# Kernel optimization log

Measured on AMD Instinct MI355X. Metric: run time of the kernel, lower is better.

## Reference

```python
import jax, jax.numpy as jnp
import numpy as np

N_NODES = 100000
NEG_SLOPE = 0.2


def _gat_conv(x, edge_index, W, att_src, att_dst, bias):
    """Single-head PyG-style GATConv with self-loops.
    x: [N, F_in], edge_index: [2, E] (row 0 = src j, row 1 = dst i).
    """
    N = x.shape[0]
    h = x @ W  # [N, F_out]
    # add self-loops
    loop = jnp.arange(N, dtype=edge_index.dtype)
    src = jnp.concatenate([edge_index[0], loop])
    dst = jnp.concatenate([edge_index[1], loop])
    # per-node attention terms, gathered per edge
    a_s = h @ att_src  # [N]
    a_d = h @ att_dst  # [N]
    e = jax.nn.leaky_relu(a_s[src] + a_d[dst], NEG_SLOPE)  # [E+N]
    # segment softmax over incoming edges of each destination
    m = jax.ops.segment_max(e, dst, num_segments=N)  # [N]
    m = jnp.where(jnp.isfinite(m), m, 0.0)
    p = jnp.exp(e - m[dst])
    denom = jax.ops.segment_sum(p, dst, num_segments=N)  # [N], >0 due to self-loops
    alpha = p / denom[dst]  # [E+N]
    # scatter-aggregate weighted source features
    out = jax.ops.segment_sum(h[src] * alpha[:, None], dst, num_segments=N)
    return out + bias


def setup_inputs() -> dict:
    key = jax.random.key(0)
    ks = jax.random.split(key, 12)
    F_in, H, C = 128, 64, 40
    x = jax.random.normal(ks[0], (N_NODES, F_in), dtype=jnp.float32)
    edge_index = jax.random.randint(ks[1], (2, 1600000), 0, N_NODES, dtype=jnp.int64)
    s1 = 1.0 / np.sqrt(F_in)
    s2 = 1.0 / np.sqrt(H)
    return {
        "x": x,
        "edge_index": edge_index,
        "W1": jax.random.uniform(ks[2], (F_in, H), jnp.float32, -s1, s1),
        "att_src1": jax.random.uniform(ks[3], (H,), jnp.float32, -s2, s2),
        "att_dst1": jax.random.uniform(ks[4], (H,), jnp.float32, -s2, s2),
        "b1": jnp.zeros((H,), jnp.float32),
        "W2": jax.random.uniform(ks[5], (H, C), jnp.float32, -s2, s2),
        "att_src2": jax.random.uniform(ks[6], (C,), jnp.float32, -1.0 / np.sqrt(C), 1.0 / np.sqrt(C)),
        "att_dst2": jax.random.uniform(ks[7], (C,), jnp.float32, -1.0 / np.sqrt(C), 1.0 / np.sqrt(C)),
        "b2": jnp.zeros((C,), jnp.float32),
    }


def reference(x, edge_index, W1, att_src1, att_dst1, b1, W2, att_src2, att_dst2, b2):
    h = _gat_conv(x, edge_index, W1, att_src1, att_dst1, b1)
    h = jax.nn.relu(h)
    # dropout is identity in eval mode
    out = _gat_conv(h, edge_index, W2, att_src2, att_dst2, b2)
    return out
```

## Files before the change

kernel.cpp:

```cpp
#include <hip/hip_runtime.h>
#include <math.h>


#define NEG_SLOPE 0.2f
#define BIN_SHIFT 8
#define BIN_NODES 256
#define MAXBINS   512
#define CAPB      4864
#define K1_CHUNK  4096
#define MAXDEG    128
#define AGG_STRIDE 132
#define XS1 136

typedef _Float16 h4_t __attribute__((ext_vector_type(4)));
typedef _Float16 h8_t __attribute__((ext_vector_type(8)));
typedef float    f16x_t __attribute__((ext_vector_type(16)));

__device__ __forceinline__ float lrelu(float v) {
    return v > 0.f ? v : NEG_SLOPE * v;
}

__global__ __launch_bounds__(256) void prep_kernel(
    const float* __restrict__ W1, const float* __restrict__ W2,
    const float* __restrict__ as1, const float* __restrict__ ad1,
    const float* __restrict__ as2, const float* __restrict__ ad2,
    _Float16* __restrict__ w1t, _Float16* __restrict__ w2t,
    float* __restrict__ u1, float* __restrict__ v1,
    int* __restrict__ bin_cursor)
{
    const int tid = threadIdx.x;
    if (blockIdx.x == 0) {
        for (int j = tid; j < MAXBINS; j += 256) bin_cursor[j] = 0;
        for (int i = tid; i < 8192; i += 256) {
            int n = i >> 7, k = i & 127;
            w1t[i] = (_Float16)W1[k * 64 + n];
        }
        if (tid < 128) {
            float su = 0.f, sv = 0.f;
            for (int n = 0; n < 64; ++n) {
                float w = W1[tid * 64 + n];
                su += w * as1[n];
                sv += w * ad1[n];
            }
            u1[tid] = su; v1[tid] = sv;
        }
    } else {
        __shared__ float u2l[64], v2l[64];
        if (tid < 64) {
            float su = 0.f, sv = 0.f;
            for (int n = 0; n < 40; ++n) {
                float w = W2[tid * 40 + n];
                su += w * as2[n];
                sv += w * ad2[n];
            }
            u2l[tid] = su; v2l[tid] = sv;
        }
        __syncthreads();
        for (int i = tid; i < 4096; i += 256) {
            int n = i >> 6, k = i & 63;
            _Float16 o = (_Float16)0.f;
            if (n < 40)       o = (_Float16)W2[k * 40 + n];
            else if (n == 40) o = (_Float16)u2l[k];
            else if (n == 41) o = (_Float16)v2l[k];
            w2t[i] = o;
        }
    }
}

__global__ __launch_bounds__(256) void gemm1_bin_kernel(
    const float* __restrict__ x, const _Float16* __restrict__ w1t,
    const float* __restrict__ u1, const float* __restrict__ v1,
    _Float16* __restrict__ h, float* __restrict__ as_, float* __restrict__ ad_,
    int N, int gb,
    const int* __restrict__ src, const int* __restrict__ dst, int E, int nbins,
    int* __restrict__ bin_cursor, int* __restrict__ binned)
{
    __shared__ __align__(16) char smem[35840];
    const int tid = threadIdx.x;

    if (blockIdx.x < gb) {
        _Float16* Xs = (_Float16*)smem;
        _Float16* Wt = (_Float16*)(smem + 17408);
        float*    Us = (float*)(smem + 34816);
        float*    Vs = (float*)(smem + 35328);
        const int lane = tid & 63;
        const int w = tid >> 6;
        const int rh = w >> 1, ch = w & 1;
        const long rowbase = (long)blockIdx.x * 64;

        {
            const int4* s4 = (const int4*)w1t;
#pragma unroll
            for (int i = 0; i < 4; ++i) {
                int f = tid + i * 256;
                int n = f >> 4, c = f & 15;
                *(int4*)&Wt[n * XS1 + c * 8] = s4[f];
            }
        }
        {
            const float4* X4 = (const float4*)x;
            const long gmax = (long)N * 32;
#pragma unroll
            for (int i = 0; i < 8; ++i) {
                int f = tid + i * 256;
                int row = f >> 5, c4 = f & 31;
                long gi = (rowbase + row) * 32 + c4;
                float4 v = (gi < gmax) ? X4[gi] : make_float4(0.f, 0.f, 0.f, 0.f);
                h4_t hv;
                hv.x = (_Float16)v.x; hv.y = (_Float16)v.y;
                hv.z = (_Float16)v.z; hv.w = (_Float16)v.w;
                *(h4_t*)&Xs[row * XS1 + c4 * 4] = hv;
            }
        }
        if (tid < 128) Us[tid] = u1[tid];
        else { int t = tid - 128; Vs[t] = v1[t]; }
        __syncthreads();

        {
            const int arow = tid >> 2, apart = tid & 3;
            const _Float16* xr = &Xs[arow * XS1 + apart * 32];
            float ps = 0.f, pd = 0.f;
#pragma unroll
            for (int k = 0; k < 32; k += 4) {
                h4_t xv = *(const h4_t*)(xr + k);
                float4 uu = *(const float4*)&Us[apart * 32 + k];
                float4 vv = *(const float4*)&Vs[apart * 32 + k];
                float x0 = (float)xv.x, x1 = (float)xv.y, x2 = (float)xv.z, x3 = (float)xv.w;
                ps += x0 * uu.x + x1 * uu.y + x2 * uu.z + x3 * uu.w;
                pd += x0 * vv.x + x1 * vv.y + x2 * vv.z + x3 * vv.w;
            }
            ps += __shfl_xor(ps, 1); ps += __shfl_xor(ps, 2);
            pd += __shfl_xor(pd, 1); pd += __shfl_xor(pd, 2);
            if (apart == 0 && rowbase + arow < N) {
                as_[rowbase + arow] = ps;
                ad_[rowbase + arow] = pd;
            }
        }

        const int m = lane & 31, khalf = lane >> 5;
        const _Float16* ax = &Xs[(rh * 32 + m) * XS1 + khalf * 8];
        const _Float16* bx = &Wt[(ch * 32 + m) * XS1 + khalf * 8];

        f16x_t acc = {};
#pragma unroll
        for (int kc = 0; kc < 8; ++kc) {
            h8_t a = *(const h8_t*)(ax + kc * 16);
            h8_t b = *(const h8_t*)(bx + kc * 16);
            acc = __builtin_amdgcn_mfma_f32_32x32x16_f16(a, b, acc, 0, 0, 0);
        }

        const int col = ch * 32 + m;
#pragma unroll
        for (int r = 0; r < 16; ++r) {
            int rowl = (r & 3) + 8 * (r >> 2) + 4 * khalf;
            long grow = rowbase + rh * 32 + rowl;
            if (grow < N) h[grow * 64 + col] = (_Float16)acc[r];
        }
    } else {
        int* hist = (int*)smem;
        int* base = (int*)(smem + 2048);
        int* lcur = (int*)(smem + 4096);
        const int e0 = (blockIdx.x - gb) * K1_CHUNK;

        int sreg[16], dreg[16];
#pragma unroll
        for (int k = 0; k < 16; ++k) {
            int e = e0 + tid + k * 256;
            bool ok = e < E;
            dreg[k] = ok ? dst[e] : -1;
            sreg[k] = ok ? src[e] : 0;
        }

        for (int j = tid; j < nbins; j += 256) hist[j] = 0;
        __syncthreads();
#pragma unroll
        for (int k = 0; k < 16; ++k)
            if (dreg[k] >= 0) atomicAdd(&hist[dreg[k] >> BIN_SHIFT], 1);
        __syncthreads();
        for (int j = tid; j < nbins; j += 256) {
            int c = hist[j];
            base[j] = (c > 0) ? atomicAdd(&bin_cursor[j], c) : 0;
            lcur[j] = 0;
        }
        __syncthreads();
#pragma unroll
        for (int k = 0; k < 16; ++k) {
            if (dreg[k] >= 0) {
                int b = dreg[k] >> BIN_SHIFT;
                int o = atomicAdd(&lcur[b], 1);
                int pos = base[b] + o;
                if (pos < CAPB)
                    binned[b * CAPB + pos] =
                        (sreg[k] << BIN_SHIFT) | (dreg[k] & (BIN_NODES - 1));
            }
        }
    }
}

__global__ __launch_bounds__(512) void fine_kernel(
    const int* __restrict__ bin_cursor, const int* __restrict__ binned,
    int* __restrict__ csr, int* __restrict__ rowptr, int N, int nbins)
{
    __shared__ int a[MAXBINS];
    __shared__ int nh[BIN_NODES];
    __shared__ int cur[BIN_NODES];
    __shared__ int sb[2];
    const int b = blockIdx.x;
    const int tid = threadIdx.x;

    int v = (tid < nbins) ? min(bin_cursor[tid], CAPB) : 0;
    a[tid] = v;
    __syncthreads();
#pragma unroll
    for (int ofs = 1; ofs < MAXBINS; ofs <<= 1) {
        int t = (tid >= ofs) ? a[tid - ofs] : 0;
        __syncthreads();
        a[tid] += t;
        __syncthreads();
    }
    if (tid == 0) {
        sb[0] = (b > 0) ? a[b - 1] : 0;
        sb[1] = a[nbins - 1];
    }

    const int cnt = min(bin_cursor[b], CAPB);
    const int nn = min(BIN_NODES, N - b * BIN_NODES);
    const int* __restrict__ brec = binned + (long)b * CAPB;

    if (tid < BIN_NODES) nh[tid] = 0;
    __syncthreads();

    for (int k = tid; k < cnt; k += 512) {
        atomicAdd(&nh[brec[k] & (BIN_NODES - 1)], 1);
    }
    __syncthreads();

    int hv = (tid < BIN_NODES) ? nh[tid] : 0;
#pragma unroll
    for (int ofs = 1; ofs < BIN_NODES; ofs <<= 1) {
        int t = (tid >= ofs && tid < BIN_NODES) ? nh[tid - ofs] : 0;
        __syncthreads();
        if (tid < BIN_NODES) nh[tid] += t;
        __syncthreads();
    }
    const int binbase = sb[0];
    if (tid < BIN_NODES) {
        int excl = nh[tid] - hv;
        if (tid < nn) rowptr[b * BIN_NODES + tid] = binbase + excl;
        cur[tid] = binbase + excl;
    }
    if (b == nbins - 1 && tid == 0) rowptr[N] = sb[1];
    __syncthreads();

    for (int k = tid; k < cnt; k += 512) {
        int rec = brec[k];
        int pos = atomicAdd(&cur[rec & (BIN_NODES - 1)], 1);
        csr[pos] = rec >> BIN_SHIFT;
    }
}

#define XS2 72
__global__ __launch_bounds__(256) void gemm2_kernel(
    const _Float16* __restrict__ hin, const _Float16* __restrict__ w2t,
    _Float16* __restrict__ h2, float* __restrict__ as_, float* __restrict__ ad_,
    int N)
{
    __shared__ __align__(16) _Float16 Xs[64 * XS2];
    __shared__ __align__(16) _Float16 Wt[64 * XS2];
    const int tid = threadIdx.x;
    const int lane = tid & 63;
    const int w = tid >> 6;
    const int rh = w >> 1, ch = w & 1;
    const long rowbase = (long)blockIdx.x * 64;

    {
        const int4* s4 = (const int4*)w2t;
#pragma unroll
        for (int i = 0; i < 2; ++i) {
            int f = tid + i * 256;
            int n = f >> 3, c = f & 7;
            *(int4*)&Wt[n * XS2 + c * 8] = s4[f];
        }
    }
    {
        const h8_t* X8 = (const h8_t*)hin;
        const long gmax = (long)N * 8;
#pragma unroll
        for (int i = 0; i < 2; ++i) {
            int f = tid + i * 256;
            int row = f >> 3, c = f & 7;
            long gi = (rowbase + row) * 8 + c;
            h8_t v = {};
            if (gi < gmax) v = X8[gi];
#pragma unroll
            for (int j = 0; j < 8; ++j) v[j] = (v[j] > (_Float16)0.f) ? v[j] : (_Float16)0.f;
            *(h8_t*)&Xs[row * XS2 + c * 8] = v;
        }
    }
    __syncthreads();

    const int m = lane & 31, khalf = lane >> 5;
    const _Float16* ax = &Xs[(rh * 32 + m) * XS2 + khalf * 8];
    const _Float16* bx = &Wt[(ch * 32 + m) * XS2 + khalf * 8];

    f16x_t acc = {};
#pragma unroll
    for (int kc = 0; kc < 4; ++kc) {
        h8_t a = *(const h8_t*)(ax + kc * 16);
        h8_t b = *(const h8_t*)(bx + kc * 16);
        acc = __builtin_amdgcn_mfma_f32_32x32x16_f16(a, b, acc, 0, 0, 0);
    }

    const int col = ch * 32 + m;
#pragma unroll
    for (int r = 0; r < 16; ++r) {
        int rowl = (r & 3) + 8 * (r >> 2) + 4 * khalf;
        long grow = rowbase + rh * 32 + rowl;
        float v = acc[r];
        if (grow < N) {
            if (col < 40)       h2[grow * 40 + col] = (_Float16)v;
            else if (col == 40) as_[grow] = v;
            else if (col == 41) ad_[grow] = v;
        }
    }
}

template<int F, typename OT>
__global__ __launch_bounds__(256) void aggregate_kernel(
    const _Float16* __restrict__ h, const float* __restrict__ as_,
    const float* __restrict__ ad_, const int* __restrict__ rowptr,
    const int* __restrict__ csr, const float* __restrict__ bias,
    OT* __restrict__ out, int N)
{
    __shared__ __align__(16) int   Ss[16 * AGG_STRIDE];
    __shared__ __align__(16) float Ps[16 * AGG_STRIDE];
    const int tid = threadIdx.x;
    const int dl  = tid >> 4;
    const int sub = tid & 15;
    const int i = blockIdx.x * 16 + dl;
    const bool alive = (i < N);

    int r0 = 0, deg = 0;
    if (alive) {
        r0 = rowptr[i];
        deg = rowptr[i + 1] - r0;
        if (deg > MAXDEG) deg = MAXDEG;
    }
    const float adi    = alive ? ad_[i] : 0.f;
    const float e_self = alive ? lrelu(as_[i] + adi) : 0.f;

    int*   __restrict__ sp = &Ss[dl * AGG_STRIDE];
    float* __restrict__ pp = &Ps[dl * AGG_STRIDE];

    float psum = 0.f;
    for (int c = sub; c < deg; c += 16) {
        int s = csr[r0 + c];
        float p = __expf(lrelu(as_[s] + adi));
        sp[c] = s;
        pp[c] = p;
        psum += p;
    }
#pragma unroll
    for (int off = 1; off < 16; off <<= 1) psum += __shfl_xor(psum, off);
    const float p_self = __expf(e_self);
    const float inv = 1.f / (psum + p_self);

    const bool act = (sub * 4 < F);
    const int  col = act ? sub * 4 : 0;
    float4 acc = make_float4(0.f, 0.f, 0.f, 0.f);

    int k = 0;
    for (; k + 8 <= deg; k += 8) {
        int4   s0 = *(const int4*)&sp[k];
        int4   s1 = *(const int4*)&sp[k + 4];
        float4 p0 = *(const float4*)&pp[k];
        float4 p1 = *(const float4*)&pp[k + 4];
        if (act) {
            h4_t hA = *(const h4_t*)&h[(long)s0.x * F + col];
            h4_t hB = *(const h4_t*)&h[(long)s0.y * F + col];
            h4_t hC = *(const h4_t*)&h[(long)s0.z * F + col];
            h4_t hD = *(const h4_t*)&h[(long)s0.w * F + col];
            h4_t hE = *(const h4_t*)&h[(long)s1.x * F + col];
            h4_t hF = *(const h4_t*)&h[(long)s1.y * F + col];
            h4_t hG = *(const h4_t*)&h[(long)s1.z * F + col];
            h4_t hH = *(const h4_t*)&h[(long)s1.w * F + col];
            acc.x += (float)hA.x * p0.x + (float)hB.x * p0.y + (float)hC.x * p0.z + (float)hD.x * p0.w
                   + (float)hE.x * p1.x + (float)hF.x * p1.y + (float)hG.x * p1.z + (float)hH.x * p1.w;
            acc.y += (float)hA.y * p0.x + (float)hB.y * p0.y + (float)hC.y * p0.z + (float)hD.y * p0.w
                   + (float)hE.y * p1.x + (float)hF.y * p1.y + (float)hG.y * p1.z + (float)hH.y * p1.w;
            acc.z += (float)hA.z * p0.x + (float)hB.z * p0.y + (float)hC.z * p0.z + (float)hD.z * p0.w
                   + (float)hE.z * p1.x + (float)hF.z * p1.y + (float)hG.z * p1.z + (float)hH.z * p1.w;
            acc.w += (float)hA.w * p0.x + (float)hB.w * p0.y + (float)hC.w * p0.z + (float)hD.w * p0.w
                   + (float)hE.w * p1.x + (float)hF.w * p1.y + (float)hG.w * p1.z + (float)hH.w * p1.w;
        }
    }
    for (; k + 4 <= deg; k += 4) {
        int4   s0 = *(const int4*)&sp[k];
        float4 p0 = *(const float4*)&pp[k];
        if (act) {
            h4_t hA = *(const h4_t*)&h[(long)s0.x * F + col];
            h4_t hB = *(const h4_t*)&h[(long)s0.y * F + col];
            h4_t hC = *(const h4_t*)&h[(long)s0.z * F + col];
            h4_t hD = *(const h4_t*)&h[(long)s0.w * F + col];
            acc.x += (float)hA.x * p0.x + (float)hB.x * p0.y + (float)hC.x * p0.z + (float)hD.x * p0.w;
            acc.y += (float)hA.y * p0.x + (float)hB.y * p0.y + (float)hC.y * p0.z + (float)hD.y * p0.w;
            acc.z += (float)hA.z * p0.x + (float)hB.z * p0.y + (float)hC.z * p0.z + (float)hD.z * p0.w;
            acc.w += (float)hA.w * p0.x + (float)hB.w * p0.y + (float)hC.w * p0.z + (float)hD.w * p0.w;
        }
    }
    for (; k < deg; ++k) {
        int   s = sp[k];
        float p = pp[k];
        if (act) {
            h4_t hv = *(const h4_t*)&h[(long)s * F + col];
            acc.x += (float)hv.x * p; acc.y += (float)hv.y * p;
            acc.z += (float)hv.z * p; acc.w += (float)hv.w * p;
        }
    }

    if (alive && act) {
        h4_t hv = *(const h4_t*)&h[(long)i * F + col];
        float4 bv = *(const float4*)&bias[col];
        float ox = (acc.x + (float)hv.x * p_self) * inv + bv.x;
        float oy = (acc.y + (float)hv.y * p_self) * inv + bv.y;
        float oz = (acc.z + (float)hv.z * p_self) * inv + bv.z;
        float ow = (acc.w + (float)hv.w * p_self) * inv + bv.w;
        if constexpr (sizeof(OT) == 4) {
            float4 o = make_float4(ox, oy, oz, ow);
            *(float4*)&out[(long)i * F + col] = o;
        } else {
            h4_t o;
            o.x = (_Float16)ox; o.y = (_Float16)oy;
            o.z = (_Float16)oz; o.w = (_Float16)ow;
            *(h4_t*)&out[(long)i * F + col] = o;
        }
    }
}

extern "C" void kernel_launch(void* const* d_in, const int* in_sizes, int n_in,
                              void* d_out, int out_size, void* d_ws, size_t ws_size,
                              hipStream_t stream) {
    const float* x    = (const float*)d_in[0];
    const int*   ei   = (const int*)d_in[1];
    const float* W1   = (const float*)d_in[2];
    const float* at_s1= (const float*)d_in[3];
    const float* at_d1= (const float*)d_in[4];
    const float* b1   = (const float*)d_in[5];
    const float* W2   = (const float*)d_in[6];
    const float* at_s2= (const float*)d_in[7];
    const float* at_d2= (const float*)d_in[8];
    const float* b2   = (const float*)d_in[9];
    float* out = (float*)d_out;

    const int N = in_sizes[0] / 128;
    const int E = in_sizes[1] / 2;
    const int nbins = (N + BIN_NODES - 1) >> BIN_SHIFT;

    char* p = (char*)d_ws;
    auto carve = [&](size_t bytes) -> void* {
        void* r = (void*)p;
        p += (bytes + 255) & ~(size_t)255;
        return r;
    };
    int*       bin_cursor = (int*)      carve((size_t)MAXBINS * 4);
    int*       binned     = (int*)      carve((size_t)nbins * CAPB * 4);
    int*       csr        = (int*)      carve((size_t)E * 4);
    int*       rowptr     = (int*)      carve((size_t)(N + 1) * 4);
    _Float16*  w1t        = (_Float16*) carve((size_t)8192 * 2);
    _Float16*  w2t        = (_Float16*) carve((size_t)4096 * 2);
    float*     u1         = (float*)    carve((size_t)128 * 4);
    float*     v1         = (float*)    carve((size_t)128 * 4);
    _Float16*  h1         = (_Float16*) carve((size_t)N * 64 * 2);
    _Float16*  agg1h      = (_Float16*) carve((size_t)N * 64 * 2);
    _Float16*  h2         = (_Float16*) carve((size_t)N * 40 * 2);
    float*     asn        = (float*)    carve((size_t)N * 4);
    float*     adn        = (float*)    carve((size_t)N * 4);

    prep_kernel<<<2, 256, 0, stream>>>(W1, W2, at_s1, at_d1, at_s2, at_d2,
                                       w1t, w2t, u1, v1, bin_cursor);

    const int gb = (N + 63) / 64;
    const int bb = (E + K1_CHUNK - 1) / K1_CHUNK;
    gemm1_bin_kernel<<<gb + bb, 256, 0, stream>>>(
        x, w1t, u1, v1, h1, asn, adn, N, gb,
        ei, ei + E, E, nbins, bin_cursor, binned);

    fine_kernel<<<nbins, 512, 0, stream>>>(bin_cursor, binned, csr, rowptr, N, nbins);

    aggregate_kernel<64, _Float16><<<(N + 15) / 16, 256, 0, stream>>>(
        h1, asn, adn, rowptr, csr, b1, agg1h, N);

    gemm2_kernel<<<(N + 63) / 64, 256, 0, stream>>>(agg1h, w2t, h2, asn, adn, N);

    aggregate_kernel<40, float><<<(N + 15) / 16, 256, 0, stream>>>(
        h2, asn, adn, rowptr, csr, b2, out, N);
}
```

Before: 233.5 us.

## Pre-swizzle weights into MFMA fragment order and stage CSR scatter in LDS

The prep kernel now writes W1 and W2 in the per-lane MFMA B-fragment order. Both GEMM kernels therefore read B operands straight from global/L2 with coalesced 16-byte loads, with no staging through shared memory. This cuts LDS use and a sync-bound copy, which may raise occupancy, at the cost of repeated global reads of small weights. Separately, fine_kernel scatters CSR entries into an LDS buffer with local offsets and then writes them out contiguously, replacing random global stores with coalesced ones. The extra ~19KB of shared memory may lower fine_kernel occupancy.

```diff
diff --git a/kernel.cpp b/kernel.cpp
--- a/kernel.cpp
+++ b/kernel.cpp
@@ -24,7 +24,7 @@
     const float* __restrict__ W1, const float* __restrict__ W2,
     const float* __restrict__ as1, const float* __restrict__ ad1,
     const float* __restrict__ as2, const float* __restrict__ ad2,
-    _Float16* __restrict__ w1t, _Float16* __restrict__ w2t,
+    _Float16* __restrict__ w1f, _Float16* __restrict__ w2f,
     float* __restrict__ u1, float* __restrict__ v1,
     int* __restrict__ bin_cursor)
 {
@@ -32,8 +32,11 @@
     if (blockIdx.x == 0) {
         for (int j = tid; j < MAXBINS; j += 256) bin_cursor[j] = 0;
         for (int i = tid; i < 8192; i += 256) {
-            int n = i >> 7, k = i & 127;
-            w1t[i] = (_Float16)W1[k * 64 + n];
+            int j = i & 7, l = (i >> 3) & 63, q = i >> 9;
+            int kc = q & 7, ch = q >> 3;
+            int n = ch * 32 + (l & 31);
+            int k = (l >> 5) * 8 + kc * 16 + j;
+            w1f[i] = (_Float16)W1[k * 64 + n];
         }
         if (tid < 128) {
             float su = 0.f, sv = 0.f;
@@ -57,46 +60,39 @@
         }
         __syncthreads();
         for (int i = tid; i < 4096; i += 256) {
-            int n = i >> 6, k = i & 63;
+            int j = i & 7, l = (i >> 3) & 63, q = i >> 9;
+            int kc = q & 3, ch = q >> 2;
+            int n = ch * 32 + (l & 31);
+            int k = (l >> 5) * 8 + kc * 16 + j;
             _Float16 o = (_Float16)0.f;
             if (n < 40)       o = (_Float16)W2[k * 40 + n];
             else if (n == 40) o = (_Float16)u2l[k];
             else if (n == 41) o = (_Float16)v2l[k];
-            w2t[i] = o;
+            w2f[i] = o;
         }
     }
 }
 
 __global__ __launch_bounds__(256) void gemm1_bin_kernel(
-    const float* __restrict__ x, const _Float16* __restrict__ w1t,
+    const float* __restrict__ x, const _Float16* __restrict__ w1f,
     const float* __restrict__ u1, const float* __restrict__ v1,
     _Float16* __restrict__ h, float* __restrict__ as_, float* __restrict__ ad_,
     int N, int gb,
     const int* __restrict__ src, const int* __restrict__ dst, int E, int nbins,
     int* __restrict__ bin_cursor, int* __restrict__ binned)
 {
-    __shared__ __align__(16) char smem[35840];
+    __shared__ __align__(16) char smem[18432];
     const int tid = threadIdx.x;
 
     if (blockIdx.x < gb) {
         _Float16* Xs = (_Float16*)smem;
-        _Float16* Wt = (_Float16*)(smem + 17408);
-        float*    Us = (float*)(smem + 34816);
-        float*    Vs = (float*)(smem + 35328);
+        float*    Us = (float*)(smem + 17408);
+        float*    Vs = (float*)(smem + 17920);
         const int lane = tid & 63;
         const int w = tid >> 6;
         const int rh = w >> 1, ch = w & 1;
         const long rowbase = (long)blockIdx.x * 64;
 
-        {
-            const int4* s4 = (const int4*)w1t;
-#pragma unroll
-            for (int i = 0; i < 4; ++i) {
-                int f = tid + i * 256;
-                int n = f >> 4, c = f & 15;
-                *(int4*)&Wt[n * XS1 + c * 8] = s4[f];
-            }
-        }
         {
             const float4* X4 = (const float4*)x;
             const long gmax = (long)N * 32;
@@ -139,13 +135,13 @@
 
         const int m = lane & 31, khalf = lane >> 5;
         const _Float16* ax = &Xs[(rh * 32 + m) * XS1 + khalf * 8];
-        const _Float16* bx = &Wt[(ch * 32 + m) * XS1 + khalf * 8];
+        const h8_t* bF = (const h8_t*)w1f + ch * 8 * 64 + lane;
 
         f16x_t acc = {};
 #pragma unroll
         for (int kc = 0; kc < 8; ++kc) {
             h8_t a = *(const h8_t*)(ax + kc * 16);
-            h8_t b = *(const h8_t*)(bx + kc * 16);
+            h8_t b = bF[kc * 64];
             acc = __builtin_amdgcn_mfma_f32_32x32x16_f16(a, b, acc, 0, 0, 0);
         }
 
@@ -204,6 +200,7 @@
     __shared__ int a[MAXBINS];
     __shared__ int nh[BIN_NODES];
     __shared__ int cur[BIN_NODES];
+    __shared__ int lbuf[CAPB];
     __shared__ int sb[2];
     const int b = blockIdx.x;
     const int tid = threadIdx.x;
@@ -247,7 +244,7 @@
     if (tid < BIN_NODES) {
         int excl = nh[tid] - hv;
         if (tid < nn) rowptr[b * BIN_NODES + tid] = binbase + excl;
-        cur[tid] = binbase + excl;
+        cur[tid] = excl;
     }
     if (b == nbins - 1 && tid == 0) rowptr[N] = sb[1];
     __syncthreads();
@@ -255,33 +252,27 @@
     for (int k = tid; k < cnt; k += 512) {
         int rec = brec[k];
         int pos = atomicAdd(&cur[rec & (BIN_NODES - 1)], 1);
-        csr[pos] = rec >> BIN_SHIFT;
+        lbuf[pos] = rec >> BIN_SHIFT;
+    }
+    __syncthreads();
+    for (int t = tid; t < cnt; t += 512) {
+        csr[binbase + t] = lbuf[t];
     }
 }
 
 #define XS2 72
 __global__ __launch_bounds__(256) void gemm2_kernel(
-    const _Float16* __restrict__ hin, const _Float16* __restrict__ w2t,
+    const _Float16* __restrict__ hin, const _Float16* __restrict__ w2f,
     _Float16* __restrict__ h2, float* __restrict__ as_, float* __restrict__ ad_,
     int N)
 {
     __shared__ __align__(16) _Float16 Xs[64 * XS2];
-    __shared__ __align__(16) _Float16 Wt[64 * XS2];
     const int tid = threadIdx.x;
     const int lane = tid & 63;
     const int w = tid >> 6;
     const int rh = w >> 1, ch = w & 1;
     const long rowbase = (long)blockIdx.x * 64;
 
-    {
-        const int4* s4 = (const int4*)w2t;
-#pragma unroll
-        for (int i = 0; i < 2; ++i) {
-            int f = tid + i * 256;
-            int n = f >> 3, c = f & 7;
-            *(int4*)&Wt[n * XS2 + c * 8] = s4[f];
-        }
-    }
     {
         const h8_t* X8 = (const h8_t*)hin;
         const long gmax = (long)N * 8;
@@ -301,13 +292,13 @@
 
     const int m = lane & 31, khalf = lane >> 5;
     const _Float16* ax = &Xs[(rh * 32 + m) * XS2 + khalf * 8];
-    const _Float16* bx = &Wt[(ch * 32 + m) * XS2 + khalf * 8];
+    const h8_t* bF = (const h8_t*)w2f + ch * 4 * 64 + lane;
 
     f16x_t acc = {};
 #pragma unroll
     for (int kc = 0; kc < 4; ++kc) {
         h8_t a = *(const h8_t*)(ax + kc * 16);
-        h8_t b = *(const h8_t*)(bx + kc * 16);
+        h8_t b = bF[kc * 64];
         acc = __builtin_amdgcn_mfma_f32_32x32x16_f16(a, b, acc, 0, 0, 0);
     }
 
@@ -466,8 +457,8 @@
     int*       binned     = (int*)      carve((size_t)nbins * CAPB * 4);
     int*       csr        = (int*)      carve((size_t)E * 4);
     int*       rowptr     = (int*)      carve((size_t)(N + 1) * 4);
-    _Float16*  w1t        = (_Float16*) carve((size_t)8192 * 2);
-    _Float16*  w2t        = (_Float16*) carve((size_t)4096 * 2);
+    _Float16*  w1f        = (_Float16*) carve((size_t)8192 * 2);
+    _Float16*  w2f        = (_Float16*) carve((size_t)4096 * 2);
     float*     u1         = (float*)    carve((size_t)128 * 4);
     float*     v1         = (float*)    carve((size_t)128 * 4);
     _Float16*  h1         = (_Float16*) carve((size_t)N * 64 * 2);
@@ -477,12 +468,12 @@
     float*     adn        = (float*)    carve((size_t)N * 4);
 
     prep_kernel<<<2, 256, 0, stream>>>(W1, W2, at_s1, at_d1, at_s2, at_d2,
-                                       w1t, w2t, u1, v1, bin_cursor);
+                                       w1f, w2f, u1, v1, bin_cursor);
 
     const int gb = (N + 63) / 64;
     const int bb = (E + K1_CHUNK - 1) / K1_CHUNK;
     gemm1_bin_kernel<<<gb + bb, 256, 0, stream>>>(
-        x, w1t, u1, v1, h1, asn, adn, N, gb,
+        x, w1f, u1, v1, h1, asn, adn, N, gb,
         ei, ei + E, E, nbins, bin_cursor, binned);
 
     fine_kernel<<<nbins, 512, 0, stream>>>(bin_cursor, binned, csr, rowptr, N, nbins);
@@ -490,7 +481,7 @@
     aggregate_kernel<64, _Float16><<<(N + 15) / 16, 256, 0, stream>>>(
         h1, asn, adn, rowptr, csr, b1, agg1h, N);
 
-    gemm2_kernel<<<(N + 63) / 64, 256, 0, stream>>>(agg1h, w2t, h2, asn, adn, N);
+    gemm2_kernel<<<(N + 63) / 64, 256, 0, stream>>>(agg1h, w2f, h2, asn, adn, N);
 
     aggregate_kernel<40, float><<<(N + 15) / 16, 256, 0, stream>>>(
         h2, asn, adn, rowptr, csr, b2, out, N);
```

After: 222.9 us. 4.6% less time.
